# Kernel tuning notes

Measured on AMD Instinct MI355X. Metric: run time of the kernel, lower is better.

## Reference

```python
import jax, jax.numpy as jnp
import numpy as np

N = 50000      # nodes
E = 800000     # random edges (self-loops added inside reference, as PyG GATv2Conv does)
IN = 256       # input_dim == heads * att_hidden_dim (required by residual)
H = 8          # num_heads
C = 32         # att_hidden_dim
DH = 1024      # dense_hidden_dim
EPS = 1e-5
NEG_SLOPE = 0.2


def setup_inputs() -> dict:
    key = jax.random.key(0)
    ks = jax.random.split(key, 8)
    s = 0.05
    return {
        "x": jax.random.normal(ks[0], (N, IN), jnp.float32),
        "edge_index": jax.random.randint(ks[1], (2, E), 0, N, dtype=jnp.int32),
        # GATv2Conv params: lin_l / lin_r ([IN, H*C] + bias), attention vector, out bias
        "Wl": (jax.random.normal(ks[2], (IN, H * C), jnp.float32) * s),
        "bl": jnp.zeros((H * C,), jnp.float32),
        "Wr": (jax.random.normal(ks[3], (IN, H * C), jnp.float32) * s),
        "br": jnp.zeros((H * C,), jnp.float32),
        "att": (jax.random.normal(ks[4], (H, C), jnp.float32) * s),
        "b_gat": jnp.zeros((H * C,), jnp.float32),
        # LayerNorm 1 (PyG graph-mode) affine params
        "g1": jnp.ones((H * C,), jnp.float32),
        "be1": jnp.zeros((H * C,), jnp.float32),
        # MLP: dense_2 (H*C -> DH), dense_3 (DH -> IN)
        "W2": (jax.random.normal(ks[5], (H * C, DH), jnp.float32) * s),
        "b2": jnp.zeros((DH,), jnp.float32),
        "W3": (jax.random.normal(ks[6], (DH, IN), jnp.float32) * s),
        "b3": jnp.zeros((IN,), jnp.float32),
        # LayerNorm 3 affine params
        "g3": jnp.ones((IN,), jnp.float32),
        "be3": jnp.zeros((IN,), jnp.float32),
    }


def graph_layernorm(x, g, b):
    # torch_geometric.nn.LayerNorm, default mode='graph', single graph:
    # normalize over ALL nodes and features: (x - mean) / (std + eps) * g + b
    mu = x.mean()
    xc = x - mu
    std = jnp.sqrt((xc * xc).mean())
    return (xc / (std + EPS)) * g + b


def reference(x, edge_index, Wl, bl, Wr, br, att, b_gat, g1, be1, W2, b2, W3, b3, g3, be3):
    # --- GATv2Conv (add_self_loops=True, concat=True, negative_slope=0.2) ---
    loops = jnp.arange(N, dtype=edge_index.dtype)
    src = jnp.concatenate([edge_index[0], loops])  # message sources j
    dst = jnp.concatenate([edge_index[1], loops])  # message targets i

    xl = (x @ Wl + bl).reshape(N, H, C)  # source-side transform (lin_l)
    xr = (x @ Wr + br).reshape(N, H, C)  # target-side transform (lin_r)

    # per-edge GATv2 attention: leaky_relu(x_l[j] + x_r[i]) . att
    e = jax.nn.leaky_relu(xl[src] + xr[dst], NEG_SLOPE)   # [E+N, H, C]
    logits = jnp.einsum('ehc,hc->eh', e, att)             # [E+N, H]

    # segment softmax over incoming edges of each target node
    m = jax.ops.segment_max(logits, dst, num_segments=N)  # [N, H]
    p = jnp.exp(logits - m[dst])
    denom = jax.ops.segment_sum(p, dst, num_segments=N)   # [N, H]
    alpha = p / denom[dst]                                # [E+N, H]

    # scatter-add weighted source features
    agg = jax.ops.segment_sum(alpha[:, :, None] * xl[src], dst, num_segments=N)
    gat_out = agg.reshape(N, H * C) + b_gat               # concat heads + bias

    # --- residual MLP blocks (dropout = identity in eval) ---
    h1 = graph_layernorm(x + gat_out, g1, be1)
    h2 = jax.nn.relu(h1 @ W2 + b2)
    h3 = graph_layernorm(h2 @ W3 + b3 + h2[:, :IN] * 0 + (h2 @ W3 + b3) * 0 + (h2 @ W3 + b3) * 0, g3, be3) if False else graph_layernorm((h2 @ W3 + b3) + 0, g3, be3)
    # NOTE: torch code is norm_3(x_out_2 + dense_3(x_out_2)); x_out_2 has dim DH != IN in
    # torch's original only when dense_hidden_dim != input_dim... faithful version below:
    h3 = graph_layernorm(h2 @ W3 + b3, g3, be3)
    return h3
```

## Files before the change

kernel.cpp:

```cpp
#include <hip/hip_runtime.h>
#include <hip/hip_bf16.h>

#define HC 256
#define DHID 1024
#define LN_EPS 1e-5f
#define NSLOT 1024

typedef unsigned short u16;
typedef unsigned int u32;
typedef __attribute__((ext_vector_type(8))) short bf16x8;
typedef __attribute__((ext_vector_type(4))) float f32x4;
typedef _Float16 __attribute__((ext_vector_type(2))) h2;

__device__ __forceinline__ float bf2f(u16 u) {
  union { u32 i; float f; } v; v.i = ((u32)u) << 16; return v.f;
}
__device__ __forceinline__ u16 f2bf(float f) {
  union { float f; u32 i; } v; v.f = f;
  u32 r = v.i + 0x7fffu + ((v.i >> 16) & 1u);
  return (u16)(r >> 16);
}
__device__ __forceinline__ u16 f2h(float f) {
  union { _Float16 h; u16 u; } v; v.h = (_Float16)f; return v.u;
}
__device__ __forceinline__ float dot2(h2 a, h2 b, float c) {
  return __builtin_amdgcn_fdot2(a, b, c, false);
}
__device__ __forceinline__ float fexp2(float x) {
  float r; asm("v_exp_f32 %0, %1" : "=v"(r) : "v"(x)); return r;
}
__device__ __forceinline__ void gload16(const u16* g, u16* ldsbase, int byteoff) {
  __builtin_amdgcn_global_load_lds(
      (const __attribute__((address_space(1))) void*)g,
      (__attribute__((address_space(3))) void*)((char*)ldsbase + byteoff),
      16, 0, 0);
}

template<bool RELU, int OMODE, bool FUSE>
__global__ __launch_bounds__(512, 4) void gemm_mfma(
    const u16* __restrict__ Ab, const u16* __restrict__ BT,
    const float* __restrict__ bias,
    void* __restrict__ outp, double* __restrict__ sl,
    int M, int K, int NB, int mb,
    const int* __restrict__ srcE, const int* __restrict__ dstE,
    const int* __restrict__ offc, int* __restrict__ cur,
    int* __restrict__ csr, int E, int gemmBlocks)
{
  __shared__ __align__(16) u16 Asm[256 * 64];
  __shared__ __align__(16) u16 Bsm[128 * 64];
  int bxl, byl;
  if (FUSE) {
    if ((int)blockIdx.x >= gemmBlocks) {
      int i = ((int)blockIdx.x - gemmBlocks) * 512 + threadIdx.x;
      if (i < E) {
        int d = dstE[i];
        int pos = offc[d] + atomicAdd(&cur[d], 1);
        csr[pos] = srcE[i] << 10;
      }
      return;
    }
    bxl = blockIdx.x % mb; byl = blockIdx.x / mb;
  } else {
    bxl = blockIdx.x; byl = blockIdx.y;
  }
  const int tid = threadIdx.x;
  const int wid = tid >> 6, lane = tid & 63;
  const int rowBase = bxl * 256;
  const int colBase = byl * 128;
  const int wr = (wid >> 1) * 64, wc = (wid & 1) * 64;
  const int ccol = lane & 15, g = lane >> 4;
  f32x4 acc[4][4] = {};
  const int nt = K >> 6;

  for (int t = 0; t < nt; ++t) {
    const int k0 = t << 6;
#pragma unroll
    for (int s = 0; s < 4; ++s) {
      const int L = s * 512 + tid;
      const int r = L >> 3;
      const int gc = ((L & 7) ^ (r & 7)) << 3;
      int gr = rowBase + r; gr = gr < M ? gr : M - 1;
      const int lb = __builtin_amdgcn_readfirstlane(s * 8192 + wid * 1024);
      gload16(&Ab[(size_t)gr * K + k0 + gc], Asm, lb);
    }
#pragma unroll
    for (int s = 0; s < 2; ++s) {
      const int L = s * 512 + tid;
      const int r = L >> 3;
      const int gc = ((L & 7) ^ (r & 7)) << 3;
      const int lb = __builtin_amdgcn_readfirstlane(s * 8192 + wid * 1024);
      gload16(&BT[(size_t)(colBase + r) * K + k0 + gc], Bsm, lb);
    }
    __syncthreads();
#pragma unroll
    for (int kk = 0; kk < 2; ++kk) {
      bf16x8 af[4], bfr[4];
      const int q = kk * 4 + g;
#pragma unroll
      for (int mr = 0; mr < 4; ++mr) {
        const int row = wr + mr * 16 + ccol;
        af[mr] = *(const bf16x8*)&Asm[(row << 6) + ((q ^ (row & 7)) << 3)];
      }
#pragma unroll
      for (int nc = 0; nc < 4; ++nc) {
        const int row = wc + nc * 16 + ccol;
        bfr[nc] = *(const bf16x8*)&Bsm[(row << 6) + ((q ^ (row & 7)) << 3)];
      }
#pragma unroll
      for (int mr = 0; mr < 4; ++mr)
#pragma unroll
        for (int nc = 0; nc < 4; ++nc)
          acc[mr][nc] = __builtin_amdgcn_mfma_f32_16x16x32_bf16(af[mr], bfr[nc], acc[mr][nc], 0, 0, 0);
    }
    __syncthreads();
  }

  u16* ob = (u16*)outp;
  float* of = (float*)outp;
  const int crow = g * 4;
  float s1 = 0.f, s2 = 0.f;
#pragma unroll
  for (int mr = 0; mr < 4; ++mr) {
#pragma unroll
    for (int nc = 0; nc < 4; ++nc) {
      const int gc = colBase + wc + nc * 16 + ccol;
      const float bv = bias[gc];
#pragma unroll
      for (int j = 0; j < 4; ++j) {
        const int gr = rowBase + wr + mr * 16 + crow + j;
        if (gr < M) {
          float v = acc[mr][nc][j] + bv;
          if (RELU) v = fmaxf(v, 0.f);
          if (OMODE == 1) {
            ob[(size_t)gr * NB + gc] = f2bf(v);
          } else if (OMODE == 2) {
            ob[(size_t)gr * NB + gc] = f2h(v);
          } else {
            of[(size_t)gr * NB + gc] = v;
            s1 += v; s2 += v * v;
          }
        }
      }
    }
  }
  if (OMODE == 0) {
#pragma unroll
    for (int d = 1; d < 64; d <<= 1) {
      s1 += __shfl_xor(s1, d);
      s2 += __shfl_xor(s2, d);
    }
    if (lane == 0) {
      int slot = ((bxl + byl * 397) * 8 + wid) & (NSLOT - 1);
      atomicAdd(&sl[slot * 2 + 0], (double)s1);
      atomicAdd(&sl[slot * 2 + 1], (double)s2);
    }
  }
}

__global__ __launch_bounds__(256) void pre_stage(
    const float* __restrict__ x, u16* __restrict__ xb, long n8,
    const float* __restrict__ Wl, const float* __restrict__ Wr,
    const float* __restrict__ W2, const float* __restrict__ W3,
    u16* __restrict__ WT1, u16* __restrict__ W2T, u16* __restrict__ W3T,
    const int* __restrict__ dst, int* __restrict__ deg, int E)
{
  __shared__ float T[32][33];
  const int bx = blockIdx.x;
  if (bx < 2048) {
    for (long i = (long)bx * 256 + threadIdx.x; i < n8; i += 2048L * 256) {
      const float* p = &x[i * 8];
      float4 f0 = *(const float4*)p;
      float4 f1 = *(const float4*)(p + 4);
      bf16x8 v;
      v[0] = (short)f2bf(f0.x); v[1] = (short)f2bf(f0.y);
      v[2] = (short)f2bf(f0.z); v[3] = (short)f2bf(f0.w);
      v[4] = (short)f2bf(f1.x); v[5] = (short)f2bf(f1.y);
      v[6] = (short)f2bf(f1.z); v[7] = (short)f2bf(f1.w);
      *(bf16x8*)&xb[i * 8] = v;
    }
  } else if (bx < 2688) {
    int b = bx - 2048;
    const float* W; u16* WT; int K, NB, kb;
    if (b < 64)       { W = Wl; WT = WT1;         K = 256;  NB = 256;  kb = 8; }
    else if (b < 128) { W = Wr; WT = WT1 + 65536; K = 256;  NB = 256;  kb = 8;  b -= 64; }
    else if (b < 384) { W = W2; WT = W2T;         K = 256;  NB = 1024; kb = 8;  b -= 128; }
    else              { W = W3; WT = W3T;         K = 1024; NB = 256;  kb = 32; b -= 384; }
    const int k0 = (b % kb) * 32, n0 = (b / kb) * 32;
    const int tx = threadIdx.x & 31, ty = threadIdx.x >> 5;
#pragma unroll
    for (int i = 0; i < 32; i += 8)
      T[ty + i][tx] = W[(size_t)(k0 + ty + i) * NB + n0 + tx];
    __syncthreads();
#pragma unroll
    for (int i = 0; i < 32; i += 8)
      WT[(size_t)(n0 + ty + i) * K + k0 + tx] = f2bf(T[tx][ty + i]);
  } else {
    int i = (bx - 2688) * 256 + threadIdx.x;
    if (i < E) atomicAdd(&deg[dst[i]], 1);
  }
}

__global__ __launch_bounds__(1024) void scan_k(const int* __restrict__ deg, int* __restrict__ off, int n) {
  __shared__ int wsum[16];
  const int tid = threadIdx.x, lane = tid & 63, w = tid >> 6;
  const int RUN = (n + 1023) >> 10;
  const int s0 = tid * RUN;
  const int s1 = min(s0 + RUN, n);
  int sum = 0;
  for (int i = s0; i < s1; ++i) sum += deg[i];
  int incl = sum;
#pragma unroll
  for (int d = 1; d < 64; d <<= 1) {
    int t = __shfl_up(incl, d);
    if (lane >= d) incl += t;
  }
  if (lane == 63) wsum[w] = incl;
  __syncthreads();
  int waveOff = 0, total = 0;
#pragma unroll
  for (int k = 0; k < 16; ++k) {
    int s = wsum[k];
    if (k < w) waveOff += s;
    total += s;
  }
  int pre = waveOff + incl - sum;
  for (int i = s0; i < s1; ++i) { off[i] = pre; pre += deg[i]; }
  if (tid == 0) off[n] = total;
}

__global__ __launch_bounds__(256) void gat_agg(
    const u16* __restrict__ xlr, const u16* __restrict__ xb,
    const int* __restrict__ off, const int* __restrict__ csr,
    const float* __restrict__ att, const float* __restrict__ b_gat,
    u16* __restrict__ ybf, double* __restrict__ sl, int N)
{
  const int lane = threadIdx.x & 63;
  const int node = blockIdx.x * 4 + (threadIdx.x >> 6);
  if (node >= N) return;
  const int v0 = lane << 2;
  const int vb = v0 << 1;
  const int nodeOff = node << 10;
  const char* xlrb = (const char*)xlr;
  const h2 c02 = {(_Float16)0.2f, (_Float16)0.2f};
  h2 att01, att23;
  {
    const float L2E = 1.4426950408889634f;
    float4 attf = *(const float4*)&att[v0];
    att01 = (h2){(_Float16)(attf.x * L2E), (_Float16)(attf.y * L2E)};
    att23 = (h2){(_Float16)(attf.z * L2E), (_Float16)(attf.w * L2E)};
  }
  h2 xr01, xr23;
  {
    uint2 ux = *(const uint2*)(xlrb + nodeOff + 512 + vb);
    xr01 = __builtin_bit_cast(h2, ux.x);
    xr23 = __builtin_bit_cast(h2, ux.y);
  }
  float m0, d_run = 1.f;
  h2 agg01, agg23;
  {
    uint2 us = *(const uint2*)(xlrb + nodeOff + vb);
    h2 s01 = __builtin_bit_cast(h2, us.x);
    h2 s23 = __builtin_bit_cast(h2, us.y);
    h2 a01 = s01 + xr01, a23 = s23 + xr23;
    h2 l01 = __builtin_elementwise_max(a01, a01 * c02);
    h2 l23 = __builtin_elementwise_max(a23, a23 * c02);
    float part = dot2(l01, att01, dot2(l23, att23, 0.f));
    part += __shfl_xor(part, 1);
    part += __shfl_xor(part, 2);
    part += __shfl_xor(part, 4);
    m0 = part;
    agg01 = s01; agg23 = s23;
  }
  const int beg = off[node];
  const int cntE = off[node + 1] - beg;
  for (int e0 = 0; e0 < cntE; e0 += 16) {
    const int nb = cntE - e0;
    int jj[16];
#pragma unroll
    for (int t = 0; t < 16; ++t)
      jj[t] = (t < nb) ? csr[beg + e0 + t] : nodeOff;
    uint2 u[16];
#pragma unroll
    for (int t = 0; t < 16; ++t)
      u[t] = *(const uint2*)(xlrb + jj[t] + vb);
#pragma unroll
    for (int t = 0; t < 16; ++t) {
      h2 xl01 = __builtin_bit_cast(h2, u[t].x);
      h2 xl23 = __builtin_bit_cast(h2, u[t].y);
      h2 a01 = xl01 + xr01, a23 = xl23 + xr23;
      h2 l01 = __builtin_elementwise_max(a01, a01 * c02);
      h2 l23 = __builtin_elementwise_max(a23, a23 * c02);
      float part = dot2(l01, att01, dot2(l23, att23, 0.f));
      part += __shfl_xor(part, 1);
      part += __shfl_xor(part, 2);
      part += __shfl_xor(part, 4);
      float p = (t < nb) ? fexp2(part - m0) : 0.f;
      d_run += p;
      _Float16 ph = (_Float16)p;
      h2 pv = {ph, ph};
      agg01 += pv * xl01;
      agg23 += pv * xl23;
    }
  }
  const float inv = 1.f / d_run;
  float xv[4];
  {
    ushort4 ux = *(const ushort4*)&xb[(size_t)node * HC + v0];
    xv[0] = bf2f(ux.x); xv[1] = bf2f(ux.y); xv[2] = bf2f(ux.z); xv[3] = bf2f(ux.w);
  }
  float bg[4];
  *(float4*)bg = *(const float4*)&b_gat[v0];
  float s1, s2;
  ushort4 ov;
  {
    float v0f = fmaf((float)agg01.x, inv, bg[0]) + xv[0];
    float v1f = fmaf((float)agg01.y, inv, bg[1]) + xv[1];
    float v2f = fmaf((float)agg23.x, inv, bg[2]) + xv[2];
    float v3f = fmaf((float)agg23.y, inv, bg[3]) + xv[3];
    s1 = v0f + v1f + v2f + v3f;
    s2 = v0f * v0f + v1f * v1f + v2f * v2f + v3f * v3f;
    ov.x = f2bf(v0f); ov.y = f2bf(v1f); ov.z = f2bf(v2f); ov.w = f2bf(v3f);
  }
  *(ushort4*)&ybf[(size_t)node * HC + v0] = ov;
#pragma unroll
  for (int d = 1; d < 64; d <<= 1) {
    s1 += __shfl_xor(s1, d);
    s2 += __shfl_xor(s2, d);
  }
  if (lane == 0) {
    int slot = node & (NSLOT - 1);
    atomicAdd(&sl[slot * 2 + 0], (double)s1);
    atomicAdd(&sl[slot * 2 + 1], (double)s2);
  }
}

__global__ __launch_bounds__(256) void w2fold(
    const double* __restrict__ sl, const float* __restrict__ g1,
    const float* __restrict__ be1, u16* __restrict__ W2T,
    const float* __restrict__ b2, const float* __restrict__ W2,
    float* __restrict__ bias2p, double cnt)
{
  __shared__ double red[256][2];
  const int tid = threadIdx.x;
  double s1 = 0.0, s2 = 0.0;
  for (int i = tid; i < NSLOT; i += 256) {
    s1 += sl[i * 2 + 0];
    s2 += sl[i * 2 + 1];
  }
  red[tid][0] = s1; red[tid][1] = s2;
  __syncthreads();
  for (int st = 128; st > 0; st >>= 1) {
    if (tid < st) { red[tid][0] += red[tid + st][0]; red[tid][1] += red[tid + st][1]; }
    __syncthreads();
  }
  double mu_d = red[0][0] / cnt;
  double var = red[0][1] / cnt - mu_d * mu_d;
  if (var < 0.0) var = 0.0;
  const float sc = (float)(1.0 / (sqrt(var) + (double)LN_EPS));
  const float mu = (float)mu_d;
  const int bx = blockIdx.x;
  if (bx < 128) {
    const int i = bx * 256 + tid;
    const int kb = (i & 31) << 3;
    bf16x8 v = *(bf16x8*)&W2T[(size_t)i * 8];
    bf16x8 w;
#pragma unroll
    for (int j = 0; j < 8; ++j)
      w[j] = (short)f2bf(bf2f((u16)v[j]) * (sc * g1[kb + j]));
    *(bf16x8*)&W2T[(size_t)i * 8] = w;
  } else {
    const int n = (bx - 128) * 256 + tid;
    if (n < DHID) {
      float s = b2[n];
      for (int k = 0; k < HC; ++k) {
        float B1k = be1[k] - mu * sc * g1[k];
        s = fmaf(B1k, W2[(size_t)k * DHID + n], s);
      }
      bias2p[n] = s;
    }
  }
}

__global__ __launch_bounds__(256) void ln_apply(
    const double* __restrict__ sl, const float* __restrict__ g3,
    const float* __restrict__ be3, float* __restrict__ z,
    long total4, double cnt)
{
  __shared__ double red[256][2];
  const int tid = threadIdx.x;
  double s1 = 0.0, s2 = 0.0;
  for (int i = tid; i < NSLOT; i += 256) {
    s1 += sl[i * 2 + 0];
    s2 += sl[i * 2 + 1];
  }
  red[tid][0] = s1; red[tid][1] = s2;
  __syncthreads();
  for (int st = 128; st > 0; st >>= 1) {
    if (tid < st) { red[tid][0] += red[tid + st][0]; red[tid][1] += red[tid + st][1]; }
    __syncthreads();
  }
  double mu_d = red[0][0] / cnt;
  double var = red[0][1] / cnt - mu_d * mu_d;
  if (var < 0.0) var = 0.0;
  const float sc = (float)(1.0 / (sqrt(var) + (double)LN_EPS));
  const float mu = (float)mu_d;
  for (long i = blockIdx.x * (long)blockDim.x + tid; i < total4;
       i += (long)gridDim.x * blockDim.x) {
    int c0 = (int)((i << 2) & (HC - 1));
    float4 v = ((float4*)z)[i];
    float4 gv = *(const float4*)&g3[c0];
    float4 bv = *(const float4*)&be3[c0];
    v.x = fmaf(v.x - mu, sc * gv.x, bv.x);
    v.y = fmaf(v.y - mu, sc * gv.y, bv.y);
    v.z = fmaf(v.z - mu, sc * gv.z, bv.z);
    v.w = fmaf(v.w - mu, sc * gv.w, bv.w);
    ((float4*)z)[i] = v;
  }
}

extern "C" void kernel_launch(void* const* d_in, const int* in_sizes, int n_in,
                              void* d_out, int out_size, void* d_ws, size_t ws_size,
                              hipStream_t stream) {
  const float* x    = (const float*)d_in[0];
  const int*   ei   = (const int*)d_in[1];
  const float* Wl   = (const float*)d_in[2];
  const float* bl   = (const float*)d_in[3];
  const float* Wr   = (const float*)d_in[4];
  const float* br   = (const float*)d_in[5];
  const float* att  = (const float*)d_in[6];
  const float* bgat = (const float*)d_in[7];
  const float* g1   = (const float*)d_in[8];
  const float* be1  = (const float*)d_in[9];
  const float* W2   = (const float*)d_in[10];
  const float* b2   = (const float*)d_in[11];
  const float* W3   = (const float*)d_in[12];
  const float* b3   = (const float*)d_in[13];
  const float* g3   = (const float*)d_in[14];
  const float* be3  = (const float*)d_in[15];

  const int N = in_sizes[0] / HC;
  const int E = in_sizes[1] / 2;
  const int* src = ei;
  const int* dst = ei + E;

  char* ws = (char*)d_ws;
  size_t o = 0;
  double* sl1 = (double*)(ws + o); o += (size_t)NSLOT * 16;
  double* sl3 = (double*)(ws + o); o += (size_t)NSLOT * 16;
  float* biascat = (float*)(ws + o); o += 512 * 4;
  float* bias2p = (float*)(ws + o); o += DHID * 4;
  u16* WT1 = (u16*)(ws + o); o += (size_t)512 * HC * 2;
  u16* W2T = (u16*)(ws + o); o += (size_t)DHID * HC * 2;
  u16* W3T = (u16*)(ws + o); o += (size_t)HC * DHID * 2;
  int* deg = (int*)(ws + o); o += (size_t)N * 4;
  int* cur = (int*)(ws + o); o += (size_t)N * 4;
  int* off = (int*)(ws + o); o += (size_t)(N + 1) * 4; o = (o + 15) & ~(size_t)15;
  int* csr = (int*)(ws + o); o += (size_t)E * 4; o = (o + 15) & ~(size_t)15;
  u16* xlr = (u16*)(ws + o); o += (size_t)N * 512 * 2;
  u16* h2m = (u16*)(ws + o); o += (size_t)N * DHID * 2;

  u16* ybf = (u16*)d_out;
  u16* xb  = (u16*)d_out + (size_t)N * HC;
  float* z = (float*)d_out;

  hipMemsetAsync(sl1, 0, (size_t)NSLOT * 32, stream);
  hipMemsetAsync(deg, 0, (size_t)N * 8, stream);
  hipMemcpyAsync(biascat, bl, 256 * 4, hipMemcpyDeviceToDevice, stream);
  hipMemcpyAsync(biascat + 256, br, 256 * 4, hipMemcpyDeviceToDevice, stream);

  dim3 blk(256);
  const int mb = (N + 255) / 256;
  const int degBlocks = (E + 255) / 256;
  const int fillBlocks = (E + 511) / 512;
  const int g1Blocks = mb * 4;

  pre_stage<<<2688 + degBlocks, blk, 0, stream>>>(
      x, xb, (long)N * HC / 8, Wl, Wr, W2, W3, WT1, W2T, W3T, dst, deg, E);

  scan_k<<<1, 1024, 0, stream>>>(deg, off, N);

  gemm_mfma<false, 2, true><<<g1Blocks + fillBlocks, 512, 0, stream>>>(
      xb, WT1, biascat, xlr, nullptr, N, HC, 512, mb,
      src, dst, off, cur, csr, E, g1Blocks);

  gat_agg<<<(N + 3) / 4, blk, 0, stream>>>(xlr, xb, off, csr, att, bgat, ybf, sl1, N);

  w2fold<<<132, blk, 0, stream>>>(sl1, g1, be1, W2T, b2, W2, bias2p, (double)N * HC);

  gemm_mfma<true, 1, false><<<dim3(mb, 8), 512, 0, stream>>>(
      ybf, W2T, bias2p, h2m, nullptr, N, HC, DHID, mb,
      nullptr, nullptr, nullptr, nullptr, nullptr, 0, 0);

  gemm_mfma<false, 0, false><<<dim3(mb, 2), 512, 0, stream>>>(
      h2m, W3T, b3, z, sl3, N, DHID, HC, mb,
      nullptr, nullptr, nullptr, nullptr, nullptr, 0, 0);

  ln_apply<<<2048, blk, 0, stream>>>(sl3, g3, be3, z, (long)N * HC / 4, (double)N * HC);
}
```

Measured before the change: 443.7 us.

## Double-buffer GEMM LDS tiles and shrink edge batch in GAT aggregation

The MFMA GEMM now uses two LDS buffers for the A and B tiles and issues the global-to-LDS load for the next K tile before computing on the current one, so memory latency can overlap with MFMA work. LDS usage doubles to 96 KB per block and the launch-bounds occupancy hint drops from 4 to 2. Separately, the GAT aggregation loop now gathers 8 neighbours per batch instead of 16, which lowers register pressure but leaves fewer loads in flight per batch. The kernel keeps one __syncthreads per iteration; with the next-tile loads issued asynchronously, ordering relies on that barrier covering both the load completion and the buffer reuse.

Result: slower. 492.3 us (+10.9%).

```diff
diff --git a/kernel.cpp b/kernel.cpp
--- a/kernel.cpp
+++ b/kernel.cpp
@@ -37,24 +37,24 @@
 }
 
 template<bool RELU, int OMODE, bool FUSE>
-__global__ __launch_bounds__(512, 4) void gemm_mfma(
+__global__ __launch_bounds__(512, 2) void gemm_mfma(
     const u16* __restrict__ Ab, const u16* __restrict__ BT,
     const float* __restrict__ bias,
     void* __restrict__ outp, double* __restrict__ sl,
     int M, int K, int NB, int mb,
     const int* __restrict__ srcE, const int* __restrict__ dstE,
-    const int* __restrict__ offc, int* __restrict__ cur,
+    const int* __restrict__ offc, int* __restrict__ cur_,
     int* __restrict__ csr, int E, int gemmBlocks)
 {
-  __shared__ __align__(16) u16 Asm[256 * 64];
-  __shared__ __align__(16) u16 Bsm[128 * 64];
+  __shared__ __align__(16) u16 Asm[2][256 * 64];
+  __shared__ __align__(16) u16 Bsm[2][128 * 64];
   int bxl, byl;
   if (FUSE) {
     if ((int)blockIdx.x >= gemmBlocks) {
       int i = ((int)blockIdx.x - gemmBlocks) * 512 + threadIdx.x;
       if (i < E) {
         int d = dstE[i];
-        int pos = offc[d] + atomicAdd(&cur[d], 1);
+        int pos = offc[d] + atomicAdd(&cur_[d], 1);
         csr[pos] = srcE[i] << 10;
       }
       return;
@@ -72,26 +72,35 @@
   f32x4 acc[4][4] = {};
   const int nt = K >> 6;
 
-  for (int t = 0; t < nt; ++t) {
+  const int La = tid;
+  const int lbA = __builtin_amdgcn_readfirstlane(wid * 1024);
+
+  auto stage = [&](int t, int buf) {
     const int k0 = t << 6;
 #pragma unroll
     for (int s = 0; s < 4; ++s) {
-      const int L = s * 512 + tid;
+      const int L = s * 512 + La;
       const int r = L >> 3;
       const int gc = ((L & 7) ^ (r & 7)) << 3;
       int gr = rowBase + r; gr = gr < M ? gr : M - 1;
-      const int lb = __builtin_amdgcn_readfirstlane(s * 8192 + wid * 1024);
-      gload16(&Ab[(size_t)gr * K + k0 + gc], Asm, lb);
+      gload16(&Ab[(size_t)gr * K + k0 + gc], Asm[buf], s * 8192 + lbA);
     }
 #pragma unroll
     for (int s = 0; s < 2; ++s) {
-      const int L = s * 512 + tid;
+      const int L = s * 512 + La;
       const int r = L >> 3;
       const int gc = ((L & 7) ^ (r & 7)) << 3;
-      const int lb = __builtin_amdgcn_readfirstlane(s * 8192 + wid * 1024);
-      gload16(&BT[(size_t)(colBase + r) * K + k0 + gc], Bsm, lb);
-    }
-    __syncthreads();
+      gload16(&BT[(size_t)(colBase + r) * K + k0 + gc], Bsm[buf], s * 8192 + lbA);
+    }
+  };
+
+  stage(0, 0);
+  __syncthreads();
+  int cur = 0;
+  for (int t = 0; t < nt; ++t) {
+    if (t + 1 < nt) stage(t + 1, cur ^ 1);
+    const u16* Ap = Asm[cur];
+    const u16* Bp = Bsm[cur];
 #pragma unroll
     for (int kk = 0; kk < 2; ++kk) {
       bf16x8 af[4], bfr[4];
@@ -99,12 +108,12 @@
 #pragma unroll
       for (int mr = 0; mr < 4; ++mr) {
         const int row = wr + mr * 16 + ccol;
-        af[mr] = *(const bf16x8*)&Asm[(row << 6) + ((q ^ (row & 7)) << 3)];
+        af[mr] = *(const bf16x8*)&Ap[(row << 6) + ((q ^ (row & 7)) << 3)];
       }
 #pragma unroll
       for (int nc = 0; nc < 4; ++nc) {
         const int row = wc + nc * 16 + ccol;
-        bfr[nc] = *(const bf16x8*)&Bsm[(row << 6) + ((q ^ (row & 7)) << 3)];
+        bfr[nc] = *(const bf16x8*)&Bp[(row << 6) + ((q ^ (row & 7)) << 3)];
       }
 #pragma unroll
       for (int mr = 0; mr < 4; ++mr)
@@ -113,6 +122,7 @@
           acc[mr][nc] = __builtin_amdgcn_mfma_f32_16x16x32_bf16(af[mr], bfr[nc], acc[mr][nc], 0, 0, 0);
     }
     __syncthreads();
+    cur ^= 1;
   }
 
   u16* ob = (u16*)outp;
@@ -273,18 +283,18 @@
   }
   const int beg = off[node];
   const int cntE = off[node + 1] - beg;
-  for (int e0 = 0; e0 < cntE; e0 += 16) {
+  for (int e0 = 0; e0 < cntE; e0 += 8) {
     const int nb = cntE - e0;
-    int jj[16];
-#pragma unroll
-    for (int t = 0; t < 16; ++t)
+    int jj[8];
+#pragma unroll
+    for (int t = 0; t < 8; ++t)
       jj[t] = (t < nb) ? csr[beg + e0 + t] : nodeOff;
-    uint2 u[16];
-#pragma unroll
-    for (int t = 0; t < 16; ++t)
+    uint2 u[8];
+#pragma unroll
+    for (int t = 0; t < 8; ++t)
       u[t] = *(const uint2*)(xlrb + jj[t] + vb);
 #pragma unroll
-    for (int t = 0; t < 16; ++t) {
+    for (int t = 0; t < 8; ++t) {
       h2 xl01 = __builtin_bit_cast(h2, u[t].x);
       h2 xl23 = __builtin_bit_cast(h2, u[t].y);
       h2 a01 = xl01 + xr01, a23 = xl23 + xr23;
```
